# Performance work log

Measured on AMD Instinct MI355X. Metric: run time of the kernel, lower is better.

## Reference

```python
import jax, jax.numpy as jnp
import numpy as np

TOTAL_WORDS = 10000
EMBED_LEN = 100
SEQ_LEN = 80
UNITS = 512
BATCH = 1024


def gru_layer(x_seq, Wx, Wh, b):
    """Keras GRU (reset_after=True), x_seq: [T, B, D] -> ys: [T, B, U]."""
    bi, br = b[0], b[1]  # input bias, recurrent bias, each [3U]
    U = Wh.shape[0]

    def step(h, x_t):
        gx = x_t @ Wx + bi            # [B, 3U]
        gh = h @ Wh + br              # [B, 3U]
        xz, xr, xh = gx[:, :U], gx[:, U:2 * U], gx[:, 2 * U:]
        hz, hr, hn = gh[:, :U], gh[:, U:2 * U], gh[:, 2 * U:]
        z = jax.nn.sigmoid(xz + hz)
        r = jax.nn.sigmoid(xr + hr)
        hh = jnp.tanh(xh + r * hn)
        h_new = z * h + (1.0 - z) * hh
        return h_new, h_new

    h0 = jnp.zeros((x_seq.shape[1], U), dtype=x_seq.dtype)
    _, ys = jax.lax.scan(step, h0, x_seq)
    return ys


def setup_inputs() -> dict:
    key = jax.random.key(0)
    ks = jax.random.split(key, 10)
    tokens = jax.random.randint(ks[0], (BATCH, SEQ_LEN), 0, TOTAL_WORDS, dtype=jnp.int32)
    s_e = 1.0 / np.sqrt(EMBED_LEN)
    s_u = 1.0 / np.sqrt(UNITS)
    emb = jax.random.normal(ks[1], (TOTAL_WORDS, EMBED_LEN), jnp.float32) * 0.05
    Wx1 = jax.random.normal(ks[2], (EMBED_LEN, 3 * UNITS), jnp.float32) * s_e
    Wh1 = jax.random.normal(ks[3], (UNITS, 3 * UNITS), jnp.float32) * s_u
    b1 = jnp.zeros((2, 3 * UNITS), jnp.float32)
    Wx2 = jax.random.normal(ks[4], (UNITS, 3 * UNITS), jnp.float32) * s_u
    Wh2 = jax.random.normal(ks[5], (UNITS, 3 * UNITS), jnp.float32) * s_u
    b2 = jnp.zeros((2, 3 * UNITS), jnp.float32)
    Wfc = jax.random.normal(ks[6], (UNITS, 1), jnp.float32) * s_u
    bfc = jnp.zeros((1,), jnp.float32)
    return {"tokens": tokens, "emb": emb, "Wx1": Wx1, "Wh1": Wh1, "b1": b1,
            "Wx2": Wx2, "Wh2": Wh2, "b2": b2, "Wfc": Wfc, "bfc": bfc}


def reference(tokens, emb, Wx1, Wh1, b1, Wx2, Wh2, b2, Wfc, bfc):
    x = emb[tokens]                       # [B, T, E]
    x = jnp.transpose(x, (1, 0, 2))       # [T, B, E] (scan over time)
    ys1 = gru_layer(x, Wx1, Wh1, b1)      # [T, B, U] return_sequences
    ys2 = gru_layer(ys1, Wx2, Wh2, b2)    # [T, B, U]
    h_last = ys2[-1]                      # [B, U] (last timestep only)
    logits = h_last @ Wfc + bfc           # [B, 1]
    return jax.nn.sigmoid(logits)
```

## Files before the change

kernel.cpp:

```cpp
#include <hip/hip_runtime.h>
#include <hip/hip_bf16.h>
#include <math.h>

typedef float f32x4 __attribute__((ext_vector_type(4)));
typedef int   ix4  __attribute__((ext_vector_type(4)));

#define MFMAI8(a,b,c) __builtin_amdgcn_mfma_i32_16x16x64_i8(a,b,c,0,0,0)

constexpr int BATCH = 1024, SEQ = 80, EMB = 100, U = 512;
constexpr int KC1 = 10;
constexpr int KC2 = 16;
constexpr float EMBMAX = 0.32f;
constexpr float INV127SQ = 1.f / 16129.f;

__device__ __forceinline__ float sigf_(float x) {
  return __builtin_amdgcn_rcpf(1.f + __expf(-x));
}
__device__ __forceinline__ float tanhf_(float x) {
  return fmaf(2.f, __builtin_amdgcn_rcpf(1.f + __expf(-2.f * x)), -1.f);
}

__global__ void k_colmax(const float* __restrict__ Wh1, const float* __restrict__ Wx1,
                         const float* __restrict__ Wh2, const float* __restrict__ Wx2,
                         float* __restrict__ scales) {
  int idx = blockIdx.x * 256 + threadIdx.x;
  if (idx >= 4 * 8 * 1536) return;
  int col = idx % 1536;
  int rest = idx / 1536;
  int kseg = rest & 7, m = rest >> 3;
  const float* W = (m == 0) ? Wh1 : (m == 1) ? Wx1 : (m == 2) ? Wh2 : Wx2;
  int Klim = (m == 1) ? EMB : 512;
  int k0 = kseg * 64, k1 = min(k0 + 64, Klim);
  float mx = 0.f;
  for (int k = k0; k < k1; ++k) mx = fmaxf(mx, fabsf(W[(size_t)k * 1536 + col]));
  if (k1 > k0) atomicMax((int*)&scales[m * 1536 + col], __float_as_int(mx));
}

__device__ __forceinline__ void pack_one(const float* __restrict__ WH,
                                         const float* __restrict__ WX,
                                         const float* __restrict__ scH,
                                         const float* __restrict__ scX,
                                         signed char* __restrict__ out,
                                         int KCH, int KCX, int KXr, int c) {
  int KC = KCH + KCX;
  int lane = c & 63;
  int rest = c >> 6;
  int g = rest % 3; rest /= 3;
  int kc = rest % KC;
  int u16 = rest / KC;
  int col = g * 512 + u16 * 16 + (lane & 15);
  int kl = (lane >> 4) * 16;
  float sH = 127.f / fmaxf(scH[col], 1e-12f);
  float sX = 127.f / fmaxf(scX[col], 1e-12f);
  ix4 v;
  signed char* vb = (signed char*)&v;
#pragma unroll
  for (int e = 0; e < 16; ++e) {
    int q = 0;
    if (kc < KCH) {
      int k = kc * 64 + kl + e;
      q = (int)rintf(WH[(size_t)k * 1536 + col] * sH);
    } else {
      int kx = (kc - KCH) * 64 + kl + e;
      if (kx < KXr) q = (int)rintf(WX[(size_t)kx * 1536 + col] * sX);
    }
    vb[e] = (signed char)q;
  }
  *(ix4*)(out + (size_t)c * 16) = v;
}

__global__ void k_prep(const float* __restrict__ Wh1, const float* __restrict__ Wx1,
                       const float* __restrict__ Wh2, const float* __restrict__ Wx2,
                       const float* __restrict__ scales,
                       signed char* __restrict__ wf1, signed char* __restrict__ wf2,
                       const float* __restrict__ emb, signed char* __restrict__ embq) {
  int b = blockIdx.x, tid = threadIdx.x;
  if (b < 240) {
    int c = b * 256 + tid;
    if (c < 61440) pack_one(Wh1, Wx1, scales, scales + 1536, wf1, 8, 2, EMB, c);
  } else if (b < 624) {
    int c = (b - 240) * 256 + tid;
    if (c < 98304) pack_one(Wh2, Wx2, scales + 3072, scales + 4608, wf2, 8, 8, U, c);
  } else {
    int idx = (b - 624) * 256 + tid;
    if (idx < 320000) {
      int r = idx >> 5, c4 = (idx & 31) * 4;
      char q[4];
#pragma unroll
      for (int j = 0; j < 4; ++j) {
        int c = c4 + j, v = 0;
        if (c < EMB) {
          float x = emb[r * EMB + c] * (127.f / EMBMAX);
          v = (int)rintf(fminf(127.f, fmaxf(-127.f, x)));
        }
        q[j] = (char)v;
      }
      *(int*)(embq + (size_t)r * 128 + c4) = *(int*)q;
    }
  }
}

__device__ __forceinline__ unsigned llc_read(unsigned* p) {
  unsigned v;
  asm volatile("global_load_dword %0, %1, off sc0 sc1\n\ts_waitcnt vmcnt(0)"
               : "=v"(v) : "v"(p) : "memory");
  return v;
}

__device__ __forceinline__ void bar_slow(unsigned* cnt, unsigned tgt) {
  __syncthreads();
  if (threadIdx.x == 0) {
    __builtin_amdgcn_fence(__ATOMIC_RELEASE, "agent");
    __hip_atomic_fetch_add(cnt, 1u, __ATOMIC_RELAXED, __HIP_MEMORY_SCOPE_AGENT);
    while (__hip_atomic_fetch_add(cnt, 0u, __ATOMIC_RELAXED, __HIP_MEMORY_SCOPE_AGENT) < tgt)
      __builtin_amdgcn_s_sleep(1);
    __builtin_amdgcn_fence(__ATOMIC_ACQUIRE, "agent");
  }
  __syncthreads();
}

__device__ __forceinline__ void bar_fast(unsigned* cnt, unsigned tgt) {
  asm volatile("s_waitcnt vmcnt(0)" ::: "memory");
  __syncthreads();
  if (threadIdx.x == 0) {
    __hip_atomic_fetch_add(cnt, 1u, __ATOMIC_RELAXED, __HIP_MEMORY_SCOPE_AGENT);
    while (llc_read(cnt) < tgt) __builtin_amdgcn_s_sleep(1);
    asm volatile("buffer_inv sc0\n\ts_waitcnt vmcnt(0)" ::: "memory");
  }
  __syncthreads();
}

__global__ __launch_bounds__(512, 2)
void k_gru_persist(const int* __restrict__ tokens, const signed char* __restrict__ embq,
                   const signed char* __restrict__ wf1, const signed char* __restrict__ wf2,
                   const float* __restrict__ b1, const float* __restrict__ b2,
                   const float* __restrict__ scales,
                   signed char* __restrict__ h1b0, signed char* __restrict__ h1b1,
                   signed char* __restrict__ h2b0, signed char* __restrict__ h2b1,
                   const float* __restrict__ Wfc, const float* __restrict__ bfc,
                   float* __restrict__ out, unsigned* __restrict__ bar) {
  __shared__ __attribute__((aligned(16))) signed char wt2[2 * KC2 * 3 * 1024];
  __shared__ int fastsh;

  const int bid = blockIdx.x, tid = threadIdx.x;
  const int g = bid & 15, lb = bid >> 4;
  const int r0 = g * 64;
  unsigned* cnt = bar + g * 64;
  unsigned* xslot = bar + 1024;

  {
    ix4* hz = (ix4*)(h1b0 + (size_t)bid * 8192);
    hz[tid] = (ix4){0, 0, 0, 0};
  }

  {
    const ix4* s2 = (const ix4*)(wf2 + (size_t)lb * 6144 * 16);
    ix4* d2 = (ix4*)wt2;
    for (int i = tid; i < 6144; i += 512) d2[i] = s2[i];
  }

  const int wv = tid >> 6, lane = tid & 63, ln = lane & 15, quad = lane >> 4;
  const int rt = wv >> 1, uh = wv & 1;
  const int u16 = lb * 2 + uh;
  const int rw0 = r0 + rt * 16;
  const int kq = quad * 16;

  ix4 w1[30];
  {
    const ix4* s1 = (const ix4*)(wf1 + (size_t)u16 * KC1 * 3 * 1024);
#pragma unroll
    for (int f = 0; f < 30; ++f) w1[f] = s1[f * 64 + lane];
  }
  const signed char* wt2h = wt2 + uh * (KC2 * 3 * 1024) + lane * 16;

  {
    unsigned xcc = 0;
    asm volatile("s_getreg_b32 %0, hwreg(HW_REG_XCC_ID)" : "=s"(xcc));
    if (tid == 0)
      __hip_atomic_store(&xslot[bid], xcc + 1u, __ATOMIC_RELAXED, __HIP_MEMORY_SCOPE_AGENT);
    bar_slow(cnt, 16u);
    if (tid == 0) {
      unsigned x0 = __hip_atomic_load(&xslot[g], __ATOMIC_RELAXED, __HIP_MEMORY_SCOPE_AGENT);
      int f = (x0 != 0u);
      for (int j = 1; j < 16; ++j)
        f &= (__hip_atomic_load(&xslot[g + 16 * j], __ATOMIC_RELAXED, __HIP_MEMORY_SCOPE_AGENT) == x0);
      fastsh = f;
    }
    __syncthreads();
  }
  const bool fastbar = (fastsh != 0);

  const int u = u16 * 16 + ln;
  const float* sc_h1 = scales, *sc_x1 = scales + 1536, *sc_h2 = scales + 3072, *sc_x2 = scales + 4608;
  const float fz1h = sc_h1[u] * INV127SQ,        fz1x = sc_x1[u] * (EMBMAX * INV127SQ);
  const float fr1h = sc_h1[512 + u] * INV127SQ,  fr1x = sc_x1[512 + u] * (EMBMAX * INV127SQ);
  const float fn1h = sc_h1[1024 + u] * INV127SQ, fn1x = sc_x1[1024 + u] * (EMBMAX * INV127SQ);
  const float fz2h = sc_h2[u] * INV127SQ,        fz2x = sc_x2[u] * INV127SQ;
  const float fr2h = sc_h2[512 + u] * INV127SQ,  fr2x = sc_x2[512 + u] * INV127SQ;
  const float fn2h = sc_h2[1024 + u] * INV127SQ, fn2x = sc_x2[1024 + u] * INV127SQ;
  const float bz1 = b1[u] + b1[1536 + u],       br1 = b1[512 + u] + b1[2048 + u];
  const float bn1x = b1[1024 + u],              bn1h = b1[2560 + u];
  const float bz2 = b2[u] + b2[1536 + u],       br2 = b2[512 + u] + b2[2048 + u];
  const float bn2x = b2[1024 + u],              bn2h = b2[2560 + u];
  const size_t wb8 = (size_t)(u >> 6) * 65536 + (u & 63);

  float h1st[4] = {0.f, 0.f, 0.f, 0.f};
  float h2st[4] = {0.f, 0.f, 0.f, 0.f};
  unsigned tgt = 32u;

#pragma unroll 1
  for (int s = 0; s <= SEQ; ++s) {
    const signed char* h1r = (s & 1) ? h1b0 : h1b1;
    signed char*       h1w = (s & 1) ? h1b1 : h1b0;
    const signed char* h2r = (s & 1) ? h2b1 : h2b0;
    signed char*       h2w = (s & 1) ? h2b0 : h2b1;

    ix4 z1h, z1x, r1h, r1x, n1h, n1x, z2h, z2x, r2h, r2x, n2h, n2x;
    z1h = z1x = r1h = r1x = n1h = n1x = (ix4){0, 0, 0, 0};
    z2h = z2x = r2h = r2x = n2h = n2x = (ix4){0, 0, 0, 0};

#pragma unroll
    for (int kc = 0; kc < 8; ++kc) {
      ix4 a = *(const ix4*)(h1r + (size_t)kc * 65536 + (rw0 + ln) * 64 + kq);
      z1h = MFMAI8(a, w1[kc * 3 + 0], z1h);
      r1h = MFMAI8(a, w1[kc * 3 + 1], r1h);
      n1h = MFMAI8(a, w1[kc * 3 + 2], n1h);
      z2x = MFMAI8(a, *(const ix4*)(wt2h + ((8 + kc) * 3 + 0) * 1024), z2x);
      r2x = MFMAI8(a, *(const ix4*)(wt2h + ((8 + kc) * 3 + 1) * 1024), r2x);
      n2x = MFMAI8(a, *(const ix4*)(wt2h + ((8 + kc) * 3 + 2) * 1024), n2x);
    }
#pragma unroll
    for (int kc = 0; kc < 8; ++kc) {
      ix4 a = *(const ix4*)(h2r + (size_t)kc * 65536 + (rw0 + ln) * 64 + kq);
      z2h = MFMAI8(a, *(const ix4*)(wt2h + (kc * 3 + 0) * 1024), z2h);
      r2h = MFMAI8(a, *(const ix4*)(wt2h + (kc * 3 + 1) * 1024), r2h);
      n2h = MFMAI8(a, *(const ix4*)(wt2h + (kc * 3 + 2) * 1024), n2h);
    }
    {
      int se = (s < SEQ) ? s : SEQ - 1;
      int tok = tokens[(size_t)(rw0 + ln) * SEQ + se];
#pragma unroll
      for (int kc = 0; kc < 2; ++kc) {
        ix4 a = *(const ix4*)(embq + (size_t)tok * 128 + kc * 64 + kq);
        z1x = MFMAI8(a, w1[(8 + kc) * 3 + 0], z1x);
        r1x = MFMAI8(a, w1[(8 + kc) * 3 + 1], r1x);
        n1x = MFMAI8(a, w1[(8 + kc) * 3 + 2], n1x);
      }
    }

    if (s < SEQ) {
#pragma unroll
      for (int i = 0; i < 4; ++i) {
        int row = rw0 + quad * 4 + i;
        float z = sigf_(fmaf(fz1h, (float)z1h[i], fmaf(fz1x, (float)z1x[i], bz1)));
        float r = sigf_(fmaf(fr1h, (float)r1h[i], fmaf(fr1x, (float)r1x[i], br1)));
        float hh = tanhf_(fmaf(fn1x, (float)n1x[i], bn1x) +
                          r * fmaf(fn1h, (float)n1h[i], bn1h));
        float hn = hh + z * (h1st[i] - hh);
        h1st[i] = hn;
        h1w[wb8 + (size_t)row * 64] = (signed char)(int)rintf(hn * 127.f);
      }
    }
    if (s >= 1) {
#pragma unroll
      for (int i = 0; i < 4; ++i) {
        int row = rw0 + quad * 4 + i;
        float z = sigf_(fmaf(fz2h, (float)z2h[i], fmaf(fz2x, (float)z2x[i], bz2)));
        float r = sigf_(fmaf(fr2h, (float)r2h[i], fmaf(fr2x, (float)r2x[i], br2)));
        float hh = tanhf_(fmaf(fn2x, (float)n2x[i], bn2x) +
                          r * fmaf(fn2h, (float)n2h[i], bn2h));
        float hn = hh + z * (h2st[i] - hh);
        h2st[i] = hn;
        h2w[wb8 + (size_t)row * 64] = (signed char)(int)rintf(hn * 127.f);
      }
    }

    if (fastbar) bar_fast(cnt, tgt);
    else         bar_slow(cnt, tgt);
    tgt += 16u;
  }

  if (wv < 4) {
    int row = r0 + lb * 4 + wv;
    float sfc = 0.f;
#pragma unroll
    for (int j = 0; j < 8; ++j) {
      int k = j * 64 + lane;
      sfc += (float)h2b1[(size_t)j * 65536 + row * 64 + lane] * Wfc[k];
    }
#pragma unroll
    for (int off = 32; off; off >>= 1) sfc += __shfl_down(sfc, off, 64);
    if (lane == 0) out[row] = sigf_(sfc * (1.f / 127.f) + bfc[0]);
  }
}

extern "C" void kernel_launch(void* const* d_in, const int* in_sizes, int n_in,
                              void* d_out, int out_size, void* d_ws, size_t ws_size,
                              hipStream_t stream) {
  const int*   tokens = (const int*)d_in[0];
  const float* emb = (const float*)d_in[1];
  const float* Wx1 = (const float*)d_in[2];
  const float* Wh1 = (const float*)d_in[3];
  const float* b1  = (const float*)d_in[4];
  const float* Wx2 = (const float*)d_in[5];
  const float* Wh2 = (const float*)d_in[6];
  const float* b2  = (const float*)d_in[7];
  const float* Wfc = (const float*)d_in[8];
  const float* bfc = (const float*)d_in[9];
  float* out = (float*)d_out;

  signed char* wf1  = (signed char*)d_ws;
  signed char* wf2  = wf1 + 983040;
  signed char* embq = wf2 + 1572864;
  float* scales     = (float*)(embq + 1280000);
  unsigned* bar     = (unsigned*)((signed char*)scales + 24576);
  signed char* h1b0 = (signed char*)bar + 8192;
  signed char* h1b1 = h1b0 + 524288;
  signed char* h2b0 = h1b1 + 524288;
  signed char* h2b1 = h2b0 + 524288;

  hipMemsetAsync(scales, 0, 24576 + 8192, stream);

  k_colmax<<<(4 * 8 * 1536 + 255) / 256, 256, 0, stream>>>(Wh1, Wx1, Wh2, Wx2, scales);
  k_prep<<<1874, 256, 0, stream>>>(Wh1, Wx1, Wh2, Wx2, scales, wf1, wf2, emb, embq);

  void* args[] = {(void*)&tokens, (void*)&embq, (void*)&wf1, (void*)&wf2,
                  (void*)&b1, (void*)&b2, (void*)&scales,
                  (void*)&h1b0, (void*)&h1b1, (void*)&h2b0, (void*)&h2b1,
                  (void*)&Wfc, (void*)&bfc, (void*)&out, (void*)&bar};
  hipLaunchCooperativeKernel((void*)k_gru_persist, dim3(256), dim3(512), args, 0, stream);
}
```

Baseline: 560.3 us.

## Split per-step barrier into layer-wise arrive/wait and remap groups by XCC

Replaces the single per-timestep group barrier with two split arrive/wait barriers, one for layer-1 hidden state and one for layer-2. Each block can then start layer-2 work and prefetch the next token's embedding projection while other blocks are still arriving. A global startup barrier now records each block's XCC and reassigns row groups so all 16 blocks in a group share one XCC, which lets the fast LLC-polling barrier be used whenever the distribution allows. This adds a startup grid-wide barrier and bounded spin loops that could silently break out on timeout.

Result: slower. 587.2 us (+4.8%).

```diff
diff --git a/kernel.cpp b/kernel.cpp
--- a/kernel.cpp
+++ b/kernel.cpp
@@ -100,32 +100,35 @@
   }
 }
 
-__device__ __forceinline__ unsigned llc_read(unsigned* p) {
+
+__device__ __forceinline__ unsigned llc_read(const unsigned* p) {
   unsigned v;
   asm volatile("global_load_dword %0, %1, off sc0 sc1\n\ts_waitcnt vmcnt(0)"
                : "=v"(v) : "v"(p) : "memory");
   return v;
 }
 
-__device__ __forceinline__ void bar_slow(unsigned* cnt, unsigned tgt) {
+__device__ __forceinline__ void bar_arrive(unsigned* cnt, bool fast) {
+  asm volatile("s_waitcnt vmcnt(0)" ::: "memory");
   __syncthreads();
   if (threadIdx.x == 0) {
-    __builtin_amdgcn_fence(__ATOMIC_RELEASE, "agent");
+    if (!fast) __builtin_amdgcn_fence(__ATOMIC_RELEASE, "agent");
     __hip_atomic_fetch_add(cnt, 1u, __ATOMIC_RELAXED, __HIP_MEMORY_SCOPE_AGENT);
-    while (__hip_atomic_fetch_add(cnt, 0u, __ATOMIC_RELAXED, __HIP_MEMORY_SCOPE_AGENT) < tgt)
+  }
+}
+
+__device__ __forceinline__ void bar_wait(const unsigned* cnt, unsigned tgt, bool fast) {
+  if (threadIdx.x == 0) {
+    int spin = 0;
+    while (llc_read(cnt) < tgt) {
       __builtin_amdgcn_s_sleep(1);
-    __builtin_amdgcn_fence(__ATOMIC_ACQUIRE, "agent");
-  }
-  __syncthreads();
-}
-
-__device__ __forceinline__ void bar_fast(unsigned* cnt, unsigned tgt) {
-  asm volatile("s_waitcnt vmcnt(0)" ::: "memory");
-  __syncthreads();
-  if (threadIdx.x == 0) {
-    __hip_atomic_fetch_add(cnt, 1u, __ATOMIC_RELAXED, __HIP_MEMORY_SCOPE_AGENT);
-    while (llc_read(cnt) < tgt) __builtin_amdgcn_s_sleep(1);
-    asm volatile("buffer_inv sc0\n\ts_waitcnt vmcnt(0)" ::: "memory");
+      if (++spin > (1 << 22)) break;
+    }
+    if (fast) {
+      asm volatile("buffer_inv sc0\n\ts_waitcnt vmcnt(0)" ::: "memory");
+    } else {
+      __builtin_amdgcn_fence(__ATOMIC_ACQUIRE, "agent");
+    }
   }
   __syncthreads();
 }
@@ -140,18 +143,62 @@
                    const float* __restrict__ Wfc, const float* __restrict__ bfc,
                    float* __restrict__ out, unsigned* __restrict__ bar) {
   __shared__ __attribute__((aligned(16))) signed char wt2[2 * KC2 * 3 * 1024];
-  __shared__ int fastsh;
+  __shared__ unsigned char s_x[256];
+  __shared__ int s_gl;
 
   const int bid = blockIdx.x, tid = threadIdx.x;
-  const int g = bid & 15, lb = bid >> 4;
-  const int r0 = g * 64;
-  unsigned* cnt = bar + g * 64;
-  unsigned* xslot = bar + 1024;
 
   {
     ix4* hz = (ix4*)(h1b0 + (size_t)bid * 8192);
     hz[tid] = (ix4){0, 0, 0, 0};
   }
+
+  unsigned* xslot = bar + 1024;
+  unsigned* gcnt  = bar + 1536;
+  unsigned xcc = 0;
+  asm volatile("s_getreg_b32 %0, hwreg(HW_REG_XCC_ID)" : "=s"(xcc));
+  if (tid == 0)
+    __hip_atomic_store(&xslot[bid], xcc + 1u, __ATOMIC_RELAXED, __HIP_MEMORY_SCOPE_AGENT);
+
+  __syncthreads();
+  if (tid == 0) {
+    __builtin_amdgcn_fence(__ATOMIC_RELEASE, "agent");
+    __hip_atomic_fetch_add(gcnt, 1u, __ATOMIC_RELAXED, __HIP_MEMORY_SCOPE_AGENT);
+    int spin = 0;
+    while (__hip_atomic_load(gcnt, __ATOMIC_RELAXED, __HIP_MEMORY_SCOPE_AGENT) < 256u) {
+      __builtin_amdgcn_s_sleep(8);
+      if (++spin > (1 << 24)) break;
+    }
+    __builtin_amdgcn_fence(__ATOMIC_ACQUIRE, "agent");
+  }
+  __syncthreads();
+
+  if (tid < 256)
+    s_x[tid] = (unsigned char)__hip_atomic_load(&xslot[tid], __ATOMIC_RELAXED,
+                                                __HIP_MEMORY_SCOPE_AGENT);
+  __syncthreads();
+  if (tid == 0) {
+    int cnts[8] = {0, 0, 0, 0, 0, 0, 0, 0};
+    int r = 0;
+    unsigned char mex = (unsigned char)(xcc + 1u);
+    for (int b = 0; b < 256; ++b) {
+      unsigned char v = s_x[b];
+      if (v >= 1 && v <= 8) cnts[v - 1]++;
+      if (b < bid && v == mex) r++;
+    }
+    int ok = 1;
+    for (int j = 0; j < 8; ++j) ok &= (cnts[j] == 32);
+    int gg, ll;
+    if (ok) { gg = (int)xcc * 2 + (r >> 4); ll = r & 15; }
+    else    { gg = bid & 15;                ll = bid >> 4; }
+    s_gl = (gg << 9) | (ll << 1) | ok;
+  }
+  __syncthreads();
+  const int g = s_gl >> 9, lb = (s_gl >> 1) & 15;
+  const bool fastbar = (s_gl & 1) != 0;
+  const int r0 = g * 64;
+  unsigned* cnt1 = bar + g * 64;
+  unsigned* cnt2 = bar + g * 64 + 32;
 
   {
     const ix4* s2 = (const ix4*)(wf2 + (size_t)lb * 6144 * 16);
@@ -172,23 +219,6 @@
     for (int f = 0; f < 30; ++f) w1[f] = s1[f * 64 + lane];
   }
   const signed char* wt2h = wt2 + uh * (KC2 * 3 * 1024) + lane * 16;
-
-  {
-    unsigned xcc = 0;
-    asm volatile("s_getreg_b32 %0, hwreg(HW_REG_XCC_ID)" : "=s"(xcc));
-    if (tid == 0)
-      __hip_atomic_store(&xslot[bid], xcc + 1u, __ATOMIC_RELAXED, __HIP_MEMORY_SCOPE_AGENT);
-    bar_slow(cnt, 16u);
-    if (tid == 0) {
-      unsigned x0 = __hip_atomic_load(&xslot[g], __ATOMIC_RELAXED, __HIP_MEMORY_SCOPE_AGENT);
-      int f = (x0 != 0u);
-      for (int j = 1; j < 16; ++j)
-        f &= (__hip_atomic_load(&xslot[g + 16 * j], __ATOMIC_RELAXED, __HIP_MEMORY_SCOPE_AGENT) == x0);
-      fastsh = f;
-    }
-    __syncthreads();
-  }
-  const bool fastbar = (fastsh != 0);
 
   const int u = u16 * 16 + ln;
   const float* sc_h1 = scales, *sc_x1 = scales + 1536, *sc_h2 = scales + 3072, *sc_x2 = scales + 4608;
@@ -206,7 +236,18 @@
 
   float h1st[4] = {0.f, 0.f, 0.f, 0.f};
   float h2st[4] = {0.f, 0.f, 0.f, 0.f};
-  unsigned tgt = 32u;
+
+  ix4 z1x = (ix4){0,0,0,0}, r1x = (ix4){0,0,0,0}, n1x = (ix4){0,0,0,0};
+  {
+    int tok = tokens[(size_t)(rw0 + ln) * SEQ];
+#pragma unroll
+    for (int kc = 0; kc < 2; ++kc) {
+      ix4 a = *(const ix4*)(embq + (size_t)tok * 128 + kc * 64 + kq);
+      z1x = MFMAI8(a, w1[(8 + kc) * 3 + 0], z1x);
+      r1x = MFMAI8(a, w1[(8 + kc) * 3 + 1], r1x);
+      n1x = MFMAI8(a, w1[(8 + kc) * 3 + 2], n1x);
+    }
+  }
 
 #pragma unroll 1
   for (int s = 0; s <= SEQ; ++s) {
@@ -215,10 +256,10 @@
     const signed char* h2r = (s & 1) ? h2b1 : h2b0;
     signed char*       h2w = (s & 1) ? h2b0 : h2b1;
 
-    ix4 z1h, z1x, r1h, r1x, n1h, n1x, z2h, z2x, r2h, r2x, n2h, n2x;
-    z1h = z1x = r1h = r1x = n1h = n1x = (ix4){0, 0, 0, 0};
-    z2h = z2x = r2h = r2x = n2h = n2x = (ix4){0, 0, 0, 0};
-
+    bar_wait(cnt1, 16u * (unsigned)s, fastbar);
+
+    ix4 z1h = (ix4){0,0,0,0}, r1h = (ix4){0,0,0,0}, n1h = (ix4){0,0,0,0};
+    ix4 z2x = (ix4){0,0,0,0}, r2x = (ix4){0,0,0,0}, n2x = (ix4){0,0,0,0};
 #pragma unroll
     for (int kc = 0; kc < 8; ++kc) {
       ix4 a = *(const ix4*)(h1r + (size_t)kc * 65536 + (rw0 + ln) * 64 + kq);
@@ -229,25 +270,6 @@
       r2x = MFMAI8(a, *(const ix4*)(wt2h + ((8 + kc) * 3 + 1) * 1024), r2x);
       n2x = MFMAI8(a, *(const ix4*)(wt2h + ((8 + kc) * 3 + 2) * 1024), n2x);
     }
-#pragma unroll
-    for (int kc = 0; kc < 8; ++kc) {
-      ix4 a = *(const ix4*)(h2r + (size_t)kc * 65536 + (rw0 + ln) * 64 + kq);
-      z2h = MFMAI8(a, *(const ix4*)(wt2h + (kc * 3 + 0) * 1024), z2h);
-      r2h = MFMAI8(a, *(const ix4*)(wt2h + (kc * 3 + 1) * 1024), r2h);
-      n2h = MFMAI8(a, *(const ix4*)(wt2h + (kc * 3 + 2) * 1024), n2h);
-    }
-    {
-      int se = (s < SEQ) ? s : SEQ - 1;
-      int tok = tokens[(size_t)(rw0 + ln) * SEQ + se];
-#pragma unroll
-      for (int kc = 0; kc < 2; ++kc) {
-        ix4 a = *(const ix4*)(embq + (size_t)tok * 128 + kc * 64 + kq);
-        z1x = MFMAI8(a, w1[(8 + kc) * 3 + 0], z1x);
-        r1x = MFMAI8(a, w1[(8 + kc) * 3 + 1], r1x);
-        n1x = MFMAI8(a, w1[(8 + kc) * 3 + 2], n1x);
-      }
-    }
-
     if (s < SEQ) {
 #pragma unroll
       for (int i = 0; i < 4; ++i) {
@@ -261,6 +283,18 @@
         h1w[wb8 + (size_t)row * 64] = (signed char)(int)rintf(hn * 127.f);
       }
     }
+    bar_arrive(cnt1, fastbar);
+
+    bar_wait(cnt2, 16u * (unsigned)s, fastbar);
+
+    ix4 z2h = (ix4){0,0,0,0}, r2h = (ix4){0,0,0,0}, n2h = (ix4){0,0,0,0};
+#pragma unroll
+    for (int kc = 0; kc < 8; ++kc) {
+      ix4 a = *(const ix4*)(h2r + (size_t)kc * 65536 + (rw0 + ln) * 64 + kq);
+      z2h = MFMAI8(a, *(const ix4*)(wt2h + (kc * 3 + 0) * 1024), z2h);
+      r2h = MFMAI8(a, *(const ix4*)(wt2h + (kc * 3 + 1) * 1024), r2h);
+      n2h = MFMAI8(a, *(const ix4*)(wt2h + (kc * 3 + 2) * 1024), n2h);
+    }
     if (s >= 1) {
 #pragma unroll
       for (int i = 0; i < 4; ++i) {
@@ -274,11 +308,22 @@
         h2w[wb8 + (size_t)row * 64] = (signed char)(int)rintf(hn * 127.f);
       }
     }
-
-    if (fastbar) bar_fast(cnt, tgt);
-    else         bar_slow(cnt, tgt);
-    tgt += 16u;
-  }
+    bar_arrive(cnt2, fastbar);
+
+    if (s < SEQ - 1) {
+      int tok = tokens[(size_t)(rw0 + ln) * SEQ + (s + 1)];
+      z1x = (ix4){0,0,0,0}; r1x = (ix4){0,0,0,0}; n1x = (ix4){0,0,0,0};
+#pragma unroll
+      for (int kc = 0; kc < 2; ++kc) {
+        ix4 a = *(const ix4*)(embq + (size_t)tok * 128 + kc * 64 + kq);
+        z1x = MFMAI8(a, w1[(8 + kc) * 3 + 0], z1x);
+        r1x = MFMAI8(a, w1[(8 + kc) * 3 + 1], r1x);
+        n1x = MFMAI8(a, w1[(8 + kc) * 3 + 2], n1x);
+      }
+    }
+  }
+
+  bar_wait(cnt2, 16u * (unsigned)(SEQ + 1), fastbar);
 
   if (wv < 4) {
     int row = r0 + lb * 4 + wv;
```

## Replace shared-counter group barrier with per-block flag barrier polled by a wavefront

Applied to the files above, without the earlier changes.

Replaces the per-group atomic counter barrier with per-block monotonic step flags, each on its own 128-byte line. One wavefront polls all 16 flags of the group in parallel using cache-bypassing loads and a wave-wide vote. The aim is to cut contention on a single counter and remove the serial atomic read-modify-write polling. The one-time XCC-locality check now runs behind a global startup barrier. It adds bounded spin timeouts, which could silently break synchronization if exceeded.

Measured after the change: 585.4 us. +4.5%, slower.

```diff
diff --git a/kernel.cpp b/kernel.cpp
--- a/kernel.cpp
+++ b/kernel.cpp
@@ -100,34 +100,12 @@
   }
 }
 
-__device__ __forceinline__ unsigned llc_read(unsigned* p) {
+
+__device__ __forceinline__ unsigned llc_read(const unsigned* p) {
   unsigned v;
   asm volatile("global_load_dword %0, %1, off sc0 sc1\n\ts_waitcnt vmcnt(0)"
                : "=v"(v) : "v"(p) : "memory");
   return v;
-}
-
-__device__ __forceinline__ void bar_slow(unsigned* cnt, unsigned tgt) {
-  __syncthreads();
-  if (threadIdx.x == 0) {
-    __builtin_amdgcn_fence(__ATOMIC_RELEASE, "agent");
-    __hip_atomic_fetch_add(cnt, 1u, __ATOMIC_RELAXED, __HIP_MEMORY_SCOPE_AGENT);
-    while (__hip_atomic_fetch_add(cnt, 0u, __ATOMIC_RELAXED, __HIP_MEMORY_SCOPE_AGENT) < tgt)
-      __builtin_amdgcn_s_sleep(1);
-    __builtin_amdgcn_fence(__ATOMIC_ACQUIRE, "agent");
-  }
-  __syncthreads();
-}
-
-__device__ __forceinline__ void bar_fast(unsigned* cnt, unsigned tgt) {
-  asm volatile("s_waitcnt vmcnt(0)" ::: "memory");
-  __syncthreads();
-  if (threadIdx.x == 0) {
-    __hip_atomic_fetch_add(cnt, 1u, __ATOMIC_RELAXED, __HIP_MEMORY_SCOPE_AGENT);
-    while (llc_read(cnt) < tgt) __builtin_amdgcn_s_sleep(1);
-    asm volatile("buffer_inv sc0\n\ts_waitcnt vmcnt(0)" ::: "memory");
-  }
-  __syncthreads();
 }
 
 __global__ __launch_bounds__(512, 2)
@@ -140,18 +118,52 @@
                    const float* __restrict__ Wfc, const float* __restrict__ bfc,
                    float* __restrict__ out, unsigned* __restrict__ bar) {
   __shared__ __attribute__((aligned(16))) signed char wt2[2 * KC2 * 3 * 1024];
-  __shared__ int fastsh;
+  __shared__ unsigned char s_x[256];
+  __shared__ int s_gl;
 
   const int bid = blockIdx.x, tid = threadIdx.x;
   const int g = bid & 15, lb = bid >> 4;
   const int r0 = g * 64;
-  unsigned* cnt = bar + g * 64;
-  unsigned* xslot = bar + 1024;
+  unsigned* fl  = bar + (size_t)g * 16 * 32;
+  unsigned* own = fl + (size_t)lb * 32;
 
   {
     ix4* hz = (ix4*)(h1b0 + (size_t)bid * 8192);
     hz[tid] = (ix4){0, 0, 0, 0};
   }
+
+  unsigned* xslot = bar + 8192;
+  unsigned* gcnt  = bar + 8512;
+  unsigned xcc = 0;
+  asm volatile("s_getreg_b32 %0, hwreg(HW_REG_XCC_ID)" : "=s"(xcc));
+  if (tid == 0)
+    __hip_atomic_store(&xslot[bid], xcc + 1u, __ATOMIC_RELAXED, __HIP_MEMORY_SCOPE_AGENT);
+
+  __syncthreads();
+  if (tid == 0) {
+    __builtin_amdgcn_fence(__ATOMIC_RELEASE, "agent");
+    __hip_atomic_fetch_add(gcnt, 1u, __ATOMIC_RELAXED, __HIP_MEMORY_SCOPE_AGENT);
+    int spin = 0;
+    while (__hip_atomic_load(gcnt, __ATOMIC_RELAXED, __HIP_MEMORY_SCOPE_AGENT) < 256u) {
+      __builtin_amdgcn_s_sleep(8);
+      if (++spin > (1 << 24)) break;
+    }
+    __builtin_amdgcn_fence(__ATOMIC_ACQUIRE, "agent");
+  }
+  __syncthreads();
+
+  if (tid < 256)
+    s_x[tid] = (unsigned char)__hip_atomic_load(&xslot[tid], __ATOMIC_RELAXED,
+                                                __HIP_MEMORY_SCOPE_AGENT);
+  __syncthreads();
+  if (tid == 0) {
+    unsigned char x0 = s_x[g];
+    int f = (x0 != 0);
+    for (int j = 1; j < 16; ++j) f &= (s_x[g + 16 * j] == x0);
+    s_gl = f;
+  }
+  __syncthreads();
+  const bool fastbar = (s_gl != 0);
 
   {
     const ix4* s2 = (const ix4*)(wf2 + (size_t)lb * 6144 * 16);
@@ -172,23 +184,6 @@
     for (int f = 0; f < 30; ++f) w1[f] = s1[f * 64 + lane];
   }
   const signed char* wt2h = wt2 + uh * (KC2 * 3 * 1024) + lane * 16;
-
-  {
-    unsigned xcc = 0;
-    asm volatile("s_getreg_b32 %0, hwreg(HW_REG_XCC_ID)" : "=s"(xcc));
-    if (tid == 0)
-      __hip_atomic_store(&xslot[bid], xcc + 1u, __ATOMIC_RELAXED, __HIP_MEMORY_SCOPE_AGENT);
-    bar_slow(cnt, 16u);
-    if (tid == 0) {
-      unsigned x0 = __hip_atomic_load(&xslot[g], __ATOMIC_RELAXED, __HIP_MEMORY_SCOPE_AGENT);
-      int f = (x0 != 0u);
-      for (int j = 1; j < 16; ++j)
-        f &= (__hip_atomic_load(&xslot[g + 16 * j], __ATOMIC_RELAXED, __HIP_MEMORY_SCOPE_AGENT) == x0);
-      fastsh = f;
-    }
-    __syncthreads();
-  }
-  const bool fastbar = (fastsh != 0);
 
   const int u = u16 * 16 + ln;
   const float* sc_h1 = scales, *sc_x1 = scales + 1536, *sc_h2 = scales + 3072, *sc_x2 = scales + 4608;
@@ -206,7 +201,6 @@
 
   float h1st[4] = {0.f, 0.f, 0.f, 0.f};
   float h2st[4] = {0.f, 0.f, 0.f, 0.f};
-  unsigned tgt = 32u;
 
 #pragma unroll 1
   for (int s = 0; s <= SEQ; ++s) {
@@ -275,9 +269,31 @@
       }
     }
 
-    if (fastbar) bar_fast(cnt, tgt);
-    else         bar_slow(cnt, tgt);
-    tgt += 16u;
+    asm volatile("s_waitcnt vmcnt(0)" ::: "memory");
+    __syncthreads();
+    if (tid == 0) {
+      if (!fastbar) __builtin_amdgcn_fence(__ATOMIC_RELEASE, "agent");
+      __hip_atomic_fetch_add(own, 1u, __ATOMIC_RELAXED, __HIP_MEMORY_SCOPE_AGENT);
+    }
+    if (wv == 0) {
+      const unsigned* fp = fl + (size_t)(lane & 15) * 32;
+      const unsigned tgt = (unsigned)s + 1u;
+      int spin = 0;
+      for (;;) {
+        unsigned v = llc_read(fp);
+        if (__all(v >= tgt)) break;
+        __builtin_amdgcn_s_sleep(1);
+        if (++spin > (1 << 22)) break;
+      }
+      if (lane == 0) {
+        if (fastbar) {
+          asm volatile("buffer_inv sc0\n\ts_waitcnt vmcnt(0)" ::: "memory");
+        } else {
+          __builtin_amdgcn_fence(__ATOMIC_ACQUIRE, "agent");
+        }
+      }
+    }
+    __syncthreads();
   }
 
   if (wv < 4) {
@@ -314,12 +330,12 @@
   signed char* embq = wf2 + 1572864;
   float* scales     = (float*)(embq + 1280000);
   unsigned* bar     = (unsigned*)((signed char*)scales + 24576);
-  signed char* h1b0 = (signed char*)bar + 8192;
+  signed char* h1b0 = (signed char*)bar + 36864;
   signed char* h1b1 = h1b0 + 524288;
   signed char* h2b0 = h1b1 + 524288;
   signed char* h2b1 = h2b0 + 524288;
 
-  hipMemsetAsync(scales, 0, 24576 + 8192, stream);
+  hipMemsetAsync(scales, 0, 24576 + 36864, stream);
 
   k_colmax<<<(4 * 8 * 1536 + 255) / 256, 256, 0, stream>>>(Wh1, Wx1, Wh2, Wx2, scales);
   k_prep<<<1874, 256, 0, stream>>>(Wh1, Wx1, Wh2, Wx2, scales, wf1, wf2, emb, embq);
```

## Fold weight quantization prep kernels into the persistent cooperative GRU kernel

Applied to the files above, without the earlier changes.

The column-max and int8 packing/embedding quantization kernels are merged into the persistent cooperative kernel as prologue phases separated by grid-wide atomic barriers. This removes two kernel launches and the gaps between them. In exchange the prep work now runs on only 256 blocks with grid-stride loops and adds two global barriers, and bounded spin loops are added to every barrier. The per-group barrier target starts at 16 because the old group barrier used during setup is gone.

Result: slower. 578.4 us (+3.2%).

```diff
diff --git a/kernel.cpp b/kernel.cpp
--- a/kernel.cpp
+++ b/kernel.cpp
@@ -18,22 +18,6 @@
 }
 __device__ __forceinline__ float tanhf_(float x) {
   return fmaf(2.f, __builtin_amdgcn_rcpf(1.f + __expf(-2.f * x)), -1.f);
-}
-
-__global__ void k_colmax(const float* __restrict__ Wh1, const float* __restrict__ Wx1,
-                         const float* __restrict__ Wh2, const float* __restrict__ Wx2,
-                         float* __restrict__ scales) {
-  int idx = blockIdx.x * 256 + threadIdx.x;
-  if (idx >= 4 * 8 * 1536) return;
-  int col = idx % 1536;
-  int rest = idx / 1536;
-  int kseg = rest & 7, m = rest >> 3;
-  const float* W = (m == 0) ? Wh1 : (m == 1) ? Wx1 : (m == 2) ? Wh2 : Wx2;
-  int Klim = (m == 1) ? EMB : 512;
-  int k0 = kseg * 64, k1 = min(k0 + 64, Klim);
-  float mx = 0.f;
-  for (int k = k0; k < k1; ++k) mx = fmaxf(mx, fabsf(W[(size_t)k * 1536 + col]));
-  if (k1 > k0) atomicMax((int*)&scales[m * 1536 + col], __float_as_int(mx));
 }
 
 __device__ __forceinline__ void pack_one(const float* __restrict__ WH,
@@ -69,37 +53,6 @@
   *(ix4*)(out + (size_t)c * 16) = v;
 }
 
-__global__ void k_prep(const float* __restrict__ Wh1, const float* __restrict__ Wx1,
-                       const float* __restrict__ Wh2, const float* __restrict__ Wx2,
-                       const float* __restrict__ scales,
-                       signed char* __restrict__ wf1, signed char* __restrict__ wf2,
-                       const float* __restrict__ emb, signed char* __restrict__ embq) {
-  int b = blockIdx.x, tid = threadIdx.x;
-  if (b < 240) {
-    int c = b * 256 + tid;
-    if (c < 61440) pack_one(Wh1, Wx1, scales, scales + 1536, wf1, 8, 2, EMB, c);
-  } else if (b < 624) {
-    int c = (b - 240) * 256 + tid;
-    if (c < 98304) pack_one(Wh2, Wx2, scales + 3072, scales + 4608, wf2, 8, 8, U, c);
-  } else {
-    int idx = (b - 624) * 256 + tid;
-    if (idx < 320000) {
-      int r = idx >> 5, c4 = (idx & 31) * 4;
-      char q[4];
-#pragma unroll
-      for (int j = 0; j < 4; ++j) {
-        int c = c4 + j, v = 0;
-        if (c < EMB) {
-          float x = emb[r * EMB + c] * (127.f / EMBMAX);
-          v = (int)rintf(fminf(127.f, fmaxf(-127.f, x)));
-        }
-        q[j] = (char)v;
-      }
-      *(int*)(embq + (size_t)r * 128 + c4) = *(int*)q;
-    }
-  }
-}
-
 __device__ __forceinline__ unsigned llc_read(unsigned* p) {
   unsigned v;
   asm volatile("global_load_dword %0, %1, off sc0 sc1\n\ts_waitcnt vmcnt(0)"
@@ -112,8 +65,11 @@
   if (threadIdx.x == 0) {
     __builtin_amdgcn_fence(__ATOMIC_RELEASE, "agent");
     __hip_atomic_fetch_add(cnt, 1u, __ATOMIC_RELAXED, __HIP_MEMORY_SCOPE_AGENT);
-    while (__hip_atomic_fetch_add(cnt, 0u, __ATOMIC_RELAXED, __HIP_MEMORY_SCOPE_AGENT) < tgt)
+    int spin = 0;
+    while (__hip_atomic_fetch_add(cnt, 0u, __ATOMIC_RELAXED, __HIP_MEMORY_SCOPE_AGENT) < tgt) {
       __builtin_amdgcn_s_sleep(1);
+      if (++spin > (1 << 22)) break;
+    }
     __builtin_amdgcn_fence(__ATOMIC_ACQUIRE, "agent");
   }
   __syncthreads();
@@ -124,17 +80,39 @@
   __syncthreads();
   if (threadIdx.x == 0) {
     __hip_atomic_fetch_add(cnt, 1u, __ATOMIC_RELAXED, __HIP_MEMORY_SCOPE_AGENT);
-    while (llc_read(cnt) < tgt) __builtin_amdgcn_s_sleep(1);
+    int spin = 0;
+    while (llc_read(cnt) < tgt) {
+      __builtin_amdgcn_s_sleep(1);
+      if (++spin > (1 << 22)) break;
+    }
     asm volatile("buffer_inv sc0\n\ts_waitcnt vmcnt(0)" ::: "memory");
   }
   __syncthreads();
 }
 
+__device__ __forceinline__ void bar_global(unsigned* gcnt, unsigned tgt) {
+  __syncthreads();
+  if (threadIdx.x == 0) {
+    __builtin_amdgcn_fence(__ATOMIC_RELEASE, "agent");
+    __hip_atomic_fetch_add(gcnt, 1u, __ATOMIC_RELAXED, __HIP_MEMORY_SCOPE_AGENT);
+    int spin = 0;
+    while (__hip_atomic_load(gcnt, __ATOMIC_RELAXED, __HIP_MEMORY_SCOPE_AGENT) < tgt) {
+      __builtin_amdgcn_s_sleep(8);
+      if (++spin > (1 << 24)) break;
+    }
+    __builtin_amdgcn_fence(__ATOMIC_ACQUIRE, "agent");
+  }
+  __syncthreads();
+}
+
 __global__ __launch_bounds__(512, 2)
-void k_gru_persist(const int* __restrict__ tokens, const signed char* __restrict__ embq,
-                   const signed char* __restrict__ wf1, const signed char* __restrict__ wf2,
+void k_gru_persist(const int* __restrict__ tokens, const float* __restrict__ emb,
+                   const float* __restrict__ Wh1, const float* __restrict__ Wx1,
+                   const float* __restrict__ Wh2, const float* __restrict__ Wx2,
+                   signed char* __restrict__ embq,
+                   signed char* __restrict__ wf1, signed char* __restrict__ wf2,
                    const float* __restrict__ b1, const float* __restrict__ b2,
-                   const float* __restrict__ scales,
+                   float* __restrict__ scales,
                    signed char* __restrict__ h1b0, signed char* __restrict__ h1b1,
                    signed char* __restrict__ h2b0, signed char* __restrict__ h2b1,
                    const float* __restrict__ Wfc, const float* __restrict__ bfc,
@@ -145,12 +123,65 @@
   const int bid = blockIdx.x, tid = threadIdx.x;
   const int g = bid & 15, lb = bid >> 4;
   const int r0 = g * 64;
+  const int gid = bid * 512 + tid;
   unsigned* cnt = bar + g * 64;
   unsigned* xslot = bar + 1024;
+  unsigned* gcnt  = bar + 1536;
 
   {
     ix4* hz = (ix4*)(h1b0 + (size_t)bid * 8192);
     hz[tid] = (ix4){0, 0, 0, 0};
+  }
+
+  {
+    unsigned xcc = 0;
+    asm volatile("s_getreg_b32 %0, hwreg(HW_REG_XCC_ID)" : "=s"(xcc));
+    if (tid == 0)
+      __hip_atomic_store(&xslot[bid], xcc + 1u, __ATOMIC_RELAXED, __HIP_MEMORY_SCOPE_AGENT);
+  }
+
+  if (gid < 4 * 8 * 1536) {
+    int col = gid % 1536;
+    int rest = gid / 1536;
+    int kseg = rest & 7, m = rest >> 3;
+    const float* W = (m == 0) ? Wh1 : (m == 1) ? Wx1 : (m == 2) ? Wh2 : Wx2;
+    int Klim = (m == 1) ? EMB : 512;
+    int k0 = kseg * 64, k1 = min(k0 + 64, Klim);
+    float mx = 0.f;
+    for (int k = k0; k < k1; ++k) mx = fmaxf(mx, fabsf(W[(size_t)k * 1536 + col]));
+    if (k1 > k0) atomicMax((int*)&scales[m * 1536 + col], __float_as_int(mx));
+  }
+
+  bar_global(gcnt, 256u);
+
+  if (gid < 61440) pack_one(Wh1, Wx1, scales, scales + 1536, wf1, 8, 2, EMB, gid);
+#pragma unroll 1
+  for (int c = gid; c < 98304; c += 131072)
+    pack_one(Wh2, Wx2, scales + 3072, scales + 4608, wf2, 8, 8, U, c);
+#pragma unroll 1
+  for (int idx = gid; idx < 320000; idx += 131072) {
+    int r = idx >> 5, c4 = (idx & 31) * 4;
+    char q[4];
+#pragma unroll
+    for (int j = 0; j < 4; ++j) {
+      int c = c4 + j, v = 0;
+      if (c < EMB) {
+        float x = emb[r * EMB + c] * (127.f / EMBMAX);
+        v = (int)rintf(fminf(127.f, fmaxf(-127.f, x)));
+      }
+      q[j] = (char)v;
+    }
+    *(int*)(embq + (size_t)r * 128 + c4) = *(int*)q;
+  }
+
+  bar_global(gcnt, 512u);
+
+  if (tid == 0) {
+    unsigned x0 = __hip_atomic_load(&xslot[g], __ATOMIC_RELAXED, __HIP_MEMORY_SCOPE_AGENT);
+    int f = (x0 != 0u);
+    for (int j = 1; j < 16; ++j)
+      f &= (__hip_atomic_load(&xslot[g + 16 * j], __ATOMIC_RELAXED, __HIP_MEMORY_SCOPE_AGENT) == x0);
+    fastsh = f;
   }
 
   {
@@ -172,23 +203,6 @@
     for (int f = 0; f < 30; ++f) w1[f] = s1[f * 64 + lane];
   }
   const signed char* wt2h = wt2 + uh * (KC2 * 3 * 1024) + lane * 16;
-
-  {
-    unsigned xcc = 0;
-    asm volatile("s_getreg_b32 %0, hwreg(HW_REG_XCC_ID)" : "=s"(xcc));
-    if (tid == 0)
-      __hip_atomic_store(&xslot[bid], xcc + 1u, __ATOMIC_RELAXED, __HIP_MEMORY_SCOPE_AGENT);
-    bar_slow(cnt, 16u);
-    if (tid == 0) {
-      unsigned x0 = __hip_atomic_load(&xslot[g], __ATOMIC_RELAXED, __HIP_MEMORY_SCOPE_AGENT);
-      int f = (x0 != 0u);
-      for (int j = 1; j < 16; ++j)
-        f &= (__hip_atomic_load(&xslot[g + 16 * j], __ATOMIC_RELAXED, __HIP_MEMORY_SCOPE_AGENT) == x0);
-      fastsh = f;
-    }
-    __syncthreads();
-  }
-  const bool fastbar = (fastsh != 0);
 
   const int u = u16 * 16 + ln;
   const float* sc_h1 = scales, *sc_x1 = scales + 1536, *sc_h2 = scales + 3072, *sc_x2 = scales + 4608;
@@ -204,9 +218,12 @@
   const float bn2x = b2[1024 + u],              bn2h = b2[2560 + u];
   const size_t wb8 = (size_t)(u >> 6) * 65536 + (u & 63);
 
+  __syncthreads();
+  const bool fastbar = (fastsh != 0);
+
   float h1st[4] = {0.f, 0.f, 0.f, 0.f};
   float h2st[4] = {0.f, 0.f, 0.f, 0.f};
-  unsigned tgt = 32u;
+  unsigned tgt = 16u;
 
 #pragma unroll 1
   for (int s = 0; s <= SEQ; ++s) {
@@ -321,10 +338,9 @@
 
   hipMemsetAsync(scales, 0, 24576 + 8192, stream);
 
-  k_colmax<<<(4 * 8 * 1536 + 255) / 256, 256, 0, stream>>>(Wh1, Wx1, Wh2, Wx2, scales);
-  k_prep<<<1874, 256, 0, stream>>>(Wh1, Wx1, Wh2, Wx2, scales, wf1, wf2, emb, embq);
-
-  void* args[] = {(void*)&tokens, (void*)&embq, (void*)&wf1, (void*)&wf2,
+  void* args[] = {(void*)&tokens, (void*)&emb,
+                  (void*)&Wh1, (void*)&Wx1, (void*)&Wh2, (void*)&Wx2,
+                  (void*)&embq, (void*)&wf1, (void*)&wf2,
                   (void*)&b1, (void*)&b2, (void*)&scales,
                   (void*)&h1b0, (void*)&h1b1, (void*)&h2b0, (void*)&h2b1,
                   (void*)&Wfc, (void*)&bfc, (void*)&out, (void*)&bar};
```
